# Kernel optimization log

Hardware: AMD Instinct MI355X
Metric: run time of the kernel (lower is better)

Reference implementation:

```python
import jax, jax.numpy as jnp
import numpy as np

N_Q, N_KV = 8, 16
D = 4_194_304
DROP_P = 0.1


def setup_inputs() -> dict:
    key = jax.random.key(0)
    qkv = jax.random.normal(key, (N_Q + N_KV, D), dtype=jnp.float32)
    return {"qkv": qkv}


def reference(qkv):
    # split([8, 16], dim=0)
    q = qkv[:N_Q]            # [8, D]
    kv = qkv[N_Q:]           # [16, D]
    qk = q @ kv.T            # [8, 16]
    # data-dependent per-query rsqrt scale from sum of squares
    inv_scale = jax.lax.rsqrt(jnp.sum(q * q, axis=-1, keepdims=True) + 1e-12)  # [8, 1]
    softmax_qk = jax.nn.softmax(qk * inv_scale, axis=-1)
    # dropout p=0.1 (training=True default in F.dropout); fixed key for reproducibility
    keep = jax.random.bernoulli(jax.random.key(42), 1.0 - DROP_P, softmax_qk.shape)
    return jnp.where(keep, softmax_qk / (1.0 - DROP_P), 0.0)
```

## Files before the change

### kernel.cpp

```cpp
#include <hip/hip_runtime.h>
#include <cstdint>

#define NQ 8
#define NKV 16
#define NGRP 4
#define KPG (NKV / NGRP)
#define NPB 40
#define NSUM 136
#define NXCD 8

__device__ __forceinline__ unsigned rotl32(unsigned x, int d) {
    return (x << d) | (x >> (32 - d));
}

__device__ __forceinline__ void threefry2x32(unsigned k0, unsigned k1,
                                             unsigned& x0, unsigned& x1) {
    const unsigned ks0 = k0, ks1 = k1, ks2 = k0 ^ k1 ^ 0x1BD11BDAu;
    x0 += ks0; x1 += ks1;
    x0 += x1; x1 = rotl32(x1, 13); x1 ^= x0;
    x0 += x1; x1 = rotl32(x1, 15); x1 ^= x0;
    x0 += x1; x1 = rotl32(x1, 26); x1 ^= x0;
    x0 += x1; x1 = rotl32(x1,  6); x1 ^= x0;
    x0 += ks1; x1 += ks2 + 1u;
    x0 += x1; x1 = rotl32(x1, 17); x1 ^= x0;
    x0 += x1; x1 = rotl32(x1, 29); x1 ^= x0;
    x0 += x1; x1 = rotl32(x1, 16); x1 ^= x0;
    x0 += x1; x1 = rotl32(x1, 24); x1 ^= x0;
    x0 += ks2; x1 += ks0 + 2u;
    x0 += x1; x1 = rotl32(x1, 13); x1 ^= x0;
    x0 += x1; x1 = rotl32(x1, 15); x1 ^= x0;
    x0 += x1; x1 = rotl32(x1, 26); x1 ^= x0;
    x0 += x1; x1 = rotl32(x1,  6); x1 ^= x0;
    x0 += ks0; x1 += ks1 + 3u;
    x0 += x1; x1 = rotl32(x1, 17); x1 ^= x0;
    x0 += x1; x1 = rotl32(x1, 29); x1 ^= x0;
    x0 += x1; x1 = rotl32(x1, 16); x1 ^= x0;
    x0 += x1; x1 = rotl32(x1, 24); x1 ^= x0;
    x0 += ks1; x1 += ks2 + 4u;
    x0 += x1; x1 = rotl32(x1, 13); x1 ^= x0;
    x0 += x1; x1 = rotl32(x1, 15); x1 ^= x0;
    x0 += x1; x1 = rotl32(x1, 26); x1 ^= x0;
    x0 += x1; x1 = rotl32(x1,  6); x1 ^= x0;
    x0 += ks2; x1 += ks0 + 5u;
}

__device__ __forceinline__ int jax_keep_bit(int idx) {
    unsigned x0 = 0u, x1 = (unsigned)idx;
    threefry2x32(0u, 42u, x0, x1);
    unsigned bits = x0 ^ x1;
    unsigned fb = (bits >> 9) | 0x3F800000u;
    float u = __uint_as_float(fb) - 1.0f;
    return u < 0.9f ? 1 : 0;
}

__device__ __forceinline__ float dot4(float4 a, float4 b) {
    return a.x * b.x + a.y * b.y + a.z * b.z + a.w * b.w;
}

__global__ __launch_bounds__(256, 4) void qk_partial_kernel(
    const float4* __restrict__ qkv, float* __restrict__ partial,
    unsigned D4, unsigned ncb)
{
    const int tid = threadIdx.x;
    const int w   = tid >> 6;
    const int lane = tid & 63;

    unsigned g, cb;
    if ((ncb & (NXCD - 1)) == 0) {
        const unsigned xcd = blockIdx.x & (NXCD - 1);
        const unsigned idx = blockIdx.x >> 3;
        g  = idx & (NGRP - 1);
        cb = (idx >> 2) * NXCD + xcd;
    } else {
        g  = blockIdx.x & (NGRP - 1);
        cb = blockIdx.x >> 2;
    }

    const float4* __restrict__ kbase = qkv + (size_t)(NQ + g * KPG) * D4;

    float acc[NQ][KPG];
#pragma unroll
    for (int r = 0; r < NQ; ++r)
#pragma unroll
        for (int j = 0; j < KPG; ++j) acc[r][j] = 0.f;
    float nacc[NQ];
#pragma unroll
    for (int r = 0; r < NQ; ++r) nacc[r] = 0.f;

    const unsigned stride = ncb * 256u;

    for (unsigned v = cb * 256u + tid; v < D4; v += stride) {
        float4 kv[KPG];
#pragma unroll
        for (int j = 0; j < KPG; ++j)
            kv[j] = kbase[(size_t)j * D4 + v];
        float4 qv[NQ];
#pragma unroll
        for (int r = 0; r < NQ; ++r)
            qv[r] = qkv[(size_t)r * D4 + v];

        if (g == 0) {
#pragma unroll
            for (int r = 0; r < NQ; ++r)
                nacc[r] += dot4(qv[r], qv[r]);
        }
#pragma unroll
        for (int r = 0; r < NQ; ++r)
#pragma unroll
            for (int j = 0; j < KPG; ++j)
                acc[r][j] += dot4(qv[r], kv[j]);
    }

    __shared__ float lred[4][NPB];
#pragma unroll
    for (int r = 0; r < NQ; ++r) {
#pragma unroll
        for (int j = 0; j < KPG; ++j) {
            float s = acc[r][j];
#pragma unroll
            for (int off = 32; off >= 1; off >>= 1)
                s += __shfl_xor(s, off, 64);
            if (lane == 0) lred[w][r * KPG + j] = s;
        }
    }
    if (g == 0) {
#pragma unroll
        for (int r = 0; r < NQ; ++r) {
            float s = nacc[r];
#pragma unroll
            for (int off = 32; off >= 1; off >>= 1)
                s += __shfl_xor(s, off, 64);
            if (lane == 0) lred[w][32 + r] = s;
        }
    } else if (lane == 0) {
#pragma unroll
        for (int r = 0; r < NQ; ++r) lred[w][32 + r] = 0.f;
    }
    __syncthreads();
    if (tid < NPB) {
        const float s = lred[0][tid] + lred[1][tid] + lred[2][tid] + lred[3][tid];
        partial[(size_t)(cb * NGRP + g) * NPB + tid] = s;
    }
}

__global__ __launch_bounds__(256) void reduce_kernel(
    const float* __restrict__ partial, float* __restrict__ sums, int ncb)
{
    const int s = blockIdx.x;
    int g, slot;
    if (s < 128) {
        const int r = s >> 4, j = s & 15;
        g = j >> 2; slot = r * KPG + (j & 3);
    } else {
        g = 0; slot = 32 + (s - 128);
    }

    float acc = 0.f;
    for (int cb = threadIdx.x; cb < ncb; cb += 256)
        acc += partial[(size_t)(cb * NGRP + g) * NPB + slot];

    float vsum = acc;
    for (int off = 32; off >= 1; off >>= 1)
        vsum += __shfl_xor(vsum, off, 64);

    __shared__ float red[4];
    const int w = threadIdx.x >> 6, lane = threadIdx.x & 63;
    if (lane == 0) red[w] = vsum;
    __syncthreads();
    if (threadIdx.x == 0) sums[s] = red[0] + red[1] + red[2] + red[3];
}

__global__ __launch_bounds__(128) void finalize_kernel(
    const float* __restrict__ sums, float* __restrict__ out)
{
    const int idx = threadIdx.x;
    const int r = idx >> 4;

    const float norm = sums[128 + r];
    const float inv_scale = rsqrtf(norm + 1e-12f);
    const float logit = sums[idx] * inv_scale;

    float m = logit;
    for (int off = 8; off >= 1; off >>= 1)
        m = fmaxf(m, __shfl_xor(m, off, 64));
    const float e = expf(logit - m);
    float ssum = e;
    for (int off = 8; off >= 1; off >>= 1)
        ssum += __shfl_xor(ssum, off, 64);
    const float sm = e / ssum;

    out[idx] = jax_keep_bit(idx) ? (sm / 0.9f) : 0.f;
}

extern "C" void kernel_launch(void* const* d_in, const int* in_sizes, int n_in,
                              void* d_out, int out_size, void* d_ws, size_t ws_size,
                              hipStream_t stream) {
    const float* qkv = (const float*)d_in[0];
    float* out = (float*)d_out;

    const long long total = (long long)in_sizes[0];
    const unsigned D  = (unsigned)(total / (NQ + NKV));
    const unsigned D4 = D / 4;

    float* wsf = (float*)d_ws;
    const long long cap_floats = (long long)(ws_size / 4);

    unsigned ncb = 256;
    long long need = (long long)ncb * NGRP * NPB + NSUM;
    while (need > cap_floats && ncb > 1) {
        ncb >>= 1;
        need = (long long)ncb * NGRP * NPB + NSUM;
    }

    float* partial = wsf;
    float* sums    = wsf + (long long)ncb * NGRP * NPB;

    qk_partial_kernel<<<ncb * NGRP, 256, 0, stream>>>(
        (const float4*)qkv, partial, D4, ncb);
    reduce_kernel<<<NSUM, 256, 0, stream>>>(partial, sums, (int)ncb);
    finalize_kernel<<<1, 128, 0, stream>>>(sums, out);
}
```

Measured before the change: 91.42 us.

## Fuse reduction and softmax into main kernel via last-block atomic counter

Replaces the three-kernel pipeline with one kernel. The last block to finish, found with an atomic counter, reduces the partial sums and applies the softmax and dropout. The work split also changes from a grid-stride loop to a contiguous span per block, and the partial sums are stored transposed so the final reduction can use float4 loads. This removes two kernel launches and their gaps but adds a memset, threadfences, and a serial tail reduction done by a single block.

```diff
diff --git a/kernel.cpp b/kernel.cpp
--- a/kernel.cpp
+++ b/kernel.cpp
@@ -6,7 +6,7 @@
 #define NGRP 4
 #define KPG (NKV / NGRP)
 #define NPB 40
-#define NSUM 136
+#define NSLOT (NGRP * NPB)
 #define NXCD 8
 
 __device__ __forceinline__ unsigned rotl32(unsigned x, int d) {
@@ -57,12 +57,13 @@
     return a.x * b.x + a.y * b.y + a.z * b.z + a.w * b.w;
 }
 
-__global__ __launch_bounds__(256, 4) void qk_partial_kernel(
+__global__ __launch_bounds__(256, 4) void qk_fused_kernel(
     const float4* __restrict__ qkv, float* __restrict__ partial,
-    unsigned D4, unsigned ncb)
+    unsigned* __restrict__ counter, float* __restrict__ out,
+    unsigned D4, unsigned ncb, unsigned span)
 {
-    const int tid = threadIdx.x;
-    const int w   = tid >> 6;
+    const int tid  = threadIdx.x;
+    const int w    = tid >> 6;
     const int lane = tid & 63;
 
     unsigned g, cb;
@@ -87,9 +88,10 @@
 #pragma unroll
     for (int r = 0; r < NQ; ++r) nacc[r] = 0.f;
 
-    const unsigned stride = ncb * 256u;
-
-    for (unsigned v = cb * 256u + tid; v < D4; v += stride) {
+    const unsigned vbeg = cb * span;
+    const unsigned vend = (vbeg + span < D4) ? (vbeg + span) : D4;
+
+    for (unsigned v = vbeg + tid; v < vend; v += 256u) {
         float4 kv[KPG];
 #pragma unroll
         for (int j = 0; j < KPG; ++j)
@@ -139,57 +141,53 @@
     __syncthreads();
     if (tid < NPB) {
         const float s = lred[0][tid] + lred[1][tid] + lred[2][tid] + lred[3][tid];
-        partial[(size_t)(cb * NGRP + g) * NPB + tid] = s;
-    }
-}
-
-__global__ __launch_bounds__(256) void reduce_kernel(
-    const float* __restrict__ partial, float* __restrict__ sums, int ncb)
-{
-    const int s = blockIdx.x;
-    int g, slot;
-    if (s < 128) {
-        const int r = s >> 4, j = s & 15;
-        g = j >> 2; slot = r * KPG + (j & 3);
-    } else {
-        g = 0; slot = 32 + (s - 128);
-    }
-
-    float acc = 0.f;
-    for (int cb = threadIdx.x; cb < ncb; cb += 256)
-        acc += partial[(size_t)(cb * NGRP + g) * NPB + slot];
-
-    float vsum = acc;
-    for (int off = 32; off >= 1; off >>= 1)
-        vsum += __shfl_xor(vsum, off, 64);
-
-    __shared__ float red[4];
-    const int w = threadIdx.x >> 6, lane = threadIdx.x & 63;
-    if (lane == 0) red[w] = vsum;
-    __syncthreads();
-    if (threadIdx.x == 0) sums[s] = red[0] + red[1] + red[2] + red[3];
-}
-
-__global__ __launch_bounds__(128) void finalize_kernel(
-    const float* __restrict__ sums, float* __restrict__ out)
-{
-    const int idx = threadIdx.x;
-    const int r = idx >> 4;
-
-    const float norm = sums[128 + r];
-    const float inv_scale = rsqrtf(norm + 1e-12f);
-    const float logit = sums[idx] * inv_scale;
-
-    float m = logit;
-    for (int off = 8; off >= 1; off >>= 1)
-        m = fmaxf(m, __shfl_xor(m, off, 64));
-    const float e = expf(logit - m);
-    float ssum = e;
-    for (int off = 8; off >= 1; off >>= 1)
-        ssum += __shfl_xor(ssum, off, 64);
-    const float sm = e / ssum;
-
-    out[idx] = jax_keep_bit(idx) ? (sm / 0.9f) : 0.f;
+        partial[(size_t)(g * NPB + tid) * ncb + cb] = s;
+    }
+
+    __threadfence();
+    __syncthreads();
+    __shared__ unsigned isLast;
+    if (tid == 0)
+        isLast = (atomicAdd(counter, 1u) == gridDim.x - 1u) ? 1u : 0u;
+    __syncthreads();
+    if (!isLast) return;
+    __threadfence();
+
+    __shared__ float wsum[NSLOT];
+    if (tid < NSLOT) {
+        float s = 0.f;
+        if ((ncb & 3u) == 0u) {
+            const float4* p4 =
+                (const float4*)(partial + (size_t)tid * ncb);
+            for (unsigned i = 0; i < (ncb >> 2); ++i) {
+                const float4 v = p4[i];
+                s += v.x + v.y + v.z + v.w;
+            }
+        } else {
+            for (unsigned i = 0; i < ncb; ++i)
+                s += partial[(size_t)tid * ncb + i];
+        }
+        wsum[tid] = s;
+    }
+    __syncthreads();
+
+    if (tid < 128) {
+        const int r = tid >> 4, j = tid & 15;
+        const float norm = wsum[32 + r];
+        const float inv_scale = rsqrtf(norm + 1e-12f);
+        const float logit =
+            wsum[(j >> 2) * NPB + r * KPG + (j & 3)] * inv_scale;
+
+        float m = logit;
+        for (int off = 8; off >= 1; off >>= 1)
+            m = fmaxf(m, __shfl_xor(m, off, 64));
+        const float e = expf(logit - m);
+        float ssum = e;
+        for (int off = 8; off >= 1; off >>= 1)
+            ssum += __shfl_xor(ssum, off, 64);
+
+        out[tid] = jax_keep_bit(tid) ? (e / ssum / 0.9f) : 0.f;
+    }
 }
 
 extern "C" void kernel_launch(void* const* d_in, const int* in_sizes, int n_in,
@@ -206,17 +204,15 @@
     const long long cap_floats = (long long)(ws_size / 4);
 
     unsigned ncb = 256;
-    long long need = (long long)ncb * NGRP * NPB + NSUM;
-    while (need > cap_floats && ncb > 1) {
-        ncb >>= 1;
-        need = (long long)ncb * NGRP * NPB + NSUM;
-    }
+    while ((long long)NSLOT * ncb + 64 > cap_floats && ncb > 1) ncb >>= 1;
+
+    const unsigned chunks = (D4 + 255u) / 256u;
+    const unsigned span = ((chunks + ncb - 1u) / ncb) * 256u;
 
     float* partial = wsf;
-    float* sums    = wsf + (long long)ncb * NGRP * NPB;
-
-    qk_partial_kernel<<<ncb * NGRP, 256, 0, stream>>>(
-        (const float4*)qkv, partial, D4, ncb);
-    reduce_kernel<<<NSUM, 256, 0, stream>>>(partial, sums, (int)ncb);
-    finalize_kernel<<<1, 128, 0, stream>>>(sums, out);
-}
+    unsigned* counter = (unsigned*)(wsf + (size_t)NSLOT * ncb);
+
+    hipMemsetAsync(counter, 0, sizeof(unsigned), stream);
+    qk_fused_kernel<<<ncb * NGRP, 256, 0, stream>>>(
+        (const float4*)qkv, partial, counter, out, D4, ncb, span);
+}
```

New measurement: 251.3 us. 175% more time.
